# Performance work log

Hardware: AMD Instinct MI355X
Metric: run time of the kernel (lower is better)

Reference implementation:

```python
import jax, jax.numpy as jnp
import numpy as np

DIM = 1024
T = 16384
WINDOW = 32
DIM_HEAD = 64
HEADS = DIM // DIM_HEAD  # 16
EPS = 1e-5


def setup_inputs() -> dict:
    key = jax.random.key(0)
    k1, k2, k3 = jax.random.split(key, 3)
    x = jax.random.normal(k1, (DIM, T), dtype=jnp.float32)
    w_qkv = jax.random.normal(k2, (3 * DIM, DIM), dtype=jnp.float32) / np.float32(np.sqrt(DIM))
    w_out = jax.random.normal(k3, (DIM, DIM), dtype=jnp.float32) / np.float32(np.sqrt(DIM))
    gamma = jnp.ones((DIM,), dtype=jnp.float32)
    beta = jnp.zeros((DIM,), dtype=jnp.float32)
    return {"x": x, "w_qkv": w_qkv, "w_out": w_out, "gamma": gamma, "beta": beta}


def _rotate_half(t):
    # original: split channels into (2, d/2), swap halves with negation
    d = t.shape[-1]
    return jnp.concatenate((-t[..., d // 2:], t[..., :d // 2]), axis=-1)


def reference(x, w_qkv, w_out, gamma, beta):
    C, Tn = x.shape
    xt = x.T  # (T, C)
    # LayerNorm over channel dim (eqx.nn.LayerNorm, eps=1e-5)
    mu = jnp.mean(xt, axis=-1, keepdims=True)
    var = jnp.var(xt, axis=-1, keepdims=True)
    normed = (xt - mu) * jax.lax.rsqrt(var + EPS) * gamma + beta
    # QKV projection (Linear with weight (out,in), no bias)
    qkv = normed @ w_qkv.T  # (T, 3C)
    q, k, v = jnp.split(qkv, 3, axis=-1)
    w = Tn // WINDOW
    def towin(t):  # (w n) (h d) -> h w n d
        return t.reshape(w, WINDOW, HEADS, DIM_HEAD).transpose(2, 0, 1, 3)
    q, k, v = map(towin, (q, k, v))
    # rotary pos emb over window positions (use_xpos=False -> scale == 1)
    inv_freq = 1.0 / (10000.0 ** (jnp.arange(0, DIM_HEAD, 2, dtype=jnp.float32) / DIM_HEAD))
    tpos = jnp.arange(WINDOW, dtype=jnp.float32)
    freqs = jnp.einsum('i,j->ij', tpos, inv_freq)  # (n, d/2)
    freqs = jnp.concatenate((freqs, freqs), axis=-1)  # (n, d)
    cos, sin = jnp.cos(freqs), jnp.sin(freqs)
    q = q * cos + _rotate_half(q) * sin
    k = k * cos + _rotate_half(k) * sin
    # per-head, per-window full (non-causal) attention
    scale = DIM_HEAD ** -0.5
    logits = jnp.einsum('hwnd,hwmd->hwnm', q, k) * scale
    attn = jax.nn.softmax(logits, axis=-1)
    out = jnp.einsum('hwnm,hwmd->hwnd', attn, v)
    out = out.transpose(1, 2, 0, 3).reshape(Tn, C)  # h w n d -> (w n) (h d)
    out = out @ w_out.T
    return out.T + x
```

## Files before the change

### kernel.cpp

```cpp
#include <hip/hip_runtime.h>

#define T_TOK 16384
#define C_DIM 1024

typedef float f32x4 __attribute__((ext_vector_type(4)));
typedef float f32x16 __attribute__((ext_vector_type(16)));
typedef __bf16 bf16x8 __attribute__((ext_vector_type(8)));
typedef unsigned short u16x8 __attribute__((ext_vector_type(8)));
typedef unsigned short u16x4 __attribute__((ext_vector_type(4)));

__device__ __forceinline__ unsigned short f2bf(float f) {
  union { float f; unsigned u; } v; v.f = f;
  unsigned r = v.u + 0x7fffu + ((v.u >> 16) & 1u);
  return (unsigned short)(r >> 16);
}
__device__ __forceinline__ float bf2f(unsigned short h) {
  union { unsigned u; float f; } v; v.u = ((unsigned)h) << 16;
  return v.f;
}
__device__ __forceinline__ unsigned pk2(float a, float b) {
  return (unsigned)f2bf(a) | ((unsigned)f2bf(b) << 16);
}

__global__ __launch_bounds__(256) void cvt_kernel(const float* __restrict__ in,
                                                  unsigned short* __restrict__ out, int n4) {
  int i = blockIdx.x * 256 + threadIdx.x;
  if (i >= n4) return;
  f32x4 v = *(const f32x4*)(in + (size_t)i * 4);
  u16x4 o;
#pragma unroll
  for (int j = 0; j < 4; ++j) o[j] = f2bf(v[j]);
  *(u16x4*)(out + (size_t)i * 4) = o;
}

__global__ __launch_bounds__(256) void rope_tab_kernel(float* __restrict__ tab) {
  int idx = blockIdx.x * 256 + threadIdx.x;
  if (idx >= 1024) return;
  int mm = idx >> 5, d = idx & 31;
  float invf = powf(10000.f, -(float)d * (1.f / 32.f));
  float ang = (float)mm * invf;
  float s, c;
  sincosf(ang, &s, &c);
  tab[idx * 2] = c;
  tab[idx * 2 + 1] = s;
}

__global__ __launch_bounds__(256) void ln_fused_kernel(const float* __restrict__ x,
                                                       const float* __restrict__ gamma,
                                                       const float* __restrict__ beta,
                                                       unsigned short* __restrict__ normed) {
  __shared__ float tile[1024][33];
  __shared__ float s1[8][32], s2[8][32];
  __shared__ float ms[32], rs[32];
  const int tid = threadIdx.x;
  const int t0 = blockIdx.x * 32;

  {
    const int tok = tid & 31, g = tid >> 5;
    float s = 0.f, ss = 0.f;
    const float* p = x + (size_t)(g * 128) * T_TOK + t0 + tok;
#pragma unroll 4
    for (int i = 0; i < 128; ++i) {
      float v = p[(size_t)i * T_TOK];
      tile[g * 128 + i][tok] = v;
      s += v; ss += v * v;
    }
    s1[g][tok] = s; s2[g][tok] = ss;
  }
  __syncthreads();
  if (tid < 32) {
    float S = 0.f, SS = 0.f;
#pragma unroll
    for (int g = 0; g < 8; ++g) { S += s1[g][tid]; SS += s2[g][tid]; }
    float m = S * (1.f / 1024.f);
    float var = SS * (1.f / 1024.f) - m * m;
    ms[tid] = m;
    rs[tid] = rsqrtf(var + 1e-5f);
  }
  __syncthreads();

  {
    const int tok = tid >> 3, cg = tid & 7;
    const float m = ms[tok], rr = rs[tok];
#pragma unroll
    for (int i = 0; i < 16; ++i) {
      int ch8 = cg * 8 + i * 64;
      u16x8 o;
#pragma unroll
      for (int j = 0; j < 8; ++j) {
        float v = tile[ch8 + j][tok];
        o[j] = f2bf((v - m) * rr * gamma[ch8 + j] + beta[ch8 + j]);
      }
      *(u16x8*)&normed[(size_t)(t0 + tok) * C_DIM + ch8] = o;
    }
  }
}

#define GLDS(gp, lp) \
  __builtin_amdgcn_global_load_lds((const __attribute__((address_space(1))) void*)(gp), \
                                   (__attribute__((address_space(3))) void*)(lp), 16, 0, 0)

#define BARF() do { __builtin_amdgcn_s_barrier(); asm volatile("" ::: "memory"); } while (0)
#define VMC(n) asm volatile("s_waitcnt vmcnt(" #n ")" ::: "memory")

__global__ __launch_bounds__(512, 2) void qkvattn_kernel(const unsigned short* __restrict__ A,
                                                         const unsigned short* __restrict__ Bq,
                                                         const float* __restrict__ ropeT,
                                                         unsigned short* __restrict__ aout) {
  __shared__ unsigned short arena[57344];
  unsigned short* LA = arena;
  unsigned short* LB = arena + 32768;
  unsigned short* QKl = arena;
  unsigned short* Vtl = arena + 34816;

  const int tid = threadIdx.x;
  const int w = tid >> 6, lane = tid & 63;
  const int wm = w >> 1, wn = w & 1;
  const int K = 1024, KT = 16;

  const int xcd = blockIdx.x & 7;
  const int ib = blockIdx.x >> 3;
  const int tt = xcd * 8 + (ib & 7);
  const int h = ib >> 3;
  const size_t m0 = (size_t)tt * 256;

  const int preslot = ((lane & 7) ^ (lane >> 3)) * 8;
  const unsigned short* gA = A + (m0 + w * 8 + (lane >> 3)) * (size_t)K + preslot;
  const unsigned short* gB0 = Bq + ((size_t)(0 + h * 64 + w * 8 + (lane >> 3))) * K + preslot;
  const unsigned short* gB1 = Bq + ((size_t)(1024 + h * 64 + w * 8 + (lane >> 3))) * K + preslot;
  const unsigned short* gB2 = Bq + ((size_t)(2048 + h * 64 + w * 8 + (lane >> 3))) * K + preslot;

  auto stageA4 = [&](int b, int kt) {
    const size_t k0 = (size_t)kt * 64;
    GLDS(gA + k0,                   LA + b * 16384 + (w * 8) * 64);
    GLDS(gA + (size_t)64 * K + k0,  LA + b * 16384 + (64 + w * 8) * 64);
    GLDS(gA + (size_t)128 * K + k0, LA + b * 16384 + (128 + w * 8) * 64);
    GLDS(gA + (size_t)192 * K + k0, LA + b * 16384 + (192 + w * 8) * 64);
  };
  auto stageB3 = [&](int b, int kt) {
    const size_t k0 = (size_t)kt * 64;
    GLDS(gB0 + k0, LB + b * 12288 + (w * 8) * 64);
    GLDS(gB1 + k0, LB + b * 12288 + (64 + w * 8) * 64);
    GLDS(gB2 + k0, LB + b * 12288 + (128 + w * 8) * 64);
  };

  f32x4 acc[4][6];
#pragma unroll
  for (int i = 0; i < 4; ++i)
#pragma unroll
    for (int j = 0; j < 6; ++j) acc[i][j] = (f32x4){0.f, 0.f, 0.f, 0.f};

  const int off_r = (lane & 15) * 64;
  const int slot0 = (((lane >> 4) ^ (lane & 7)) * 8);
  const int slot1 = slot0 ^ 32;

  bf16x8 aF[4][2], bF[6][2];

  stageA4(0, 0); stageB3(0, 0);
  stageA4(1, 1); stageB3(1, 1);
  VMC(7);
  BARF();

  int bb = 0;
  for (int t = 0; t < KT; ++t, bb ^= 1) {
    const unsigned short* Ab = LA + bb * 16384 + (wm * 64) * 64;
    const unsigned short* Bb = LB + bb * 12288 + (wn * 96) * 64;

#pragma unroll
    for (int mi = 0; mi < 2; ++mi) {
      aF[mi][0] = *(const bf16x8*)&Ab[mi * 1024 + off_r + slot0];
      aF[mi][1] = *(const bf16x8*)&Ab[mi * 1024 + off_r + slot1];
    }
#pragma unroll
    for (int ni = 0; ni < 6; ++ni) {
      bF[ni][0] = *(const bf16x8*)&Bb[ni * 1024 + off_r + slot0];
      bF[ni][1] = *(const bf16x8*)&Bb[ni * 1024 + off_r + slot1];
    }

    __builtin_amdgcn_s_setprio(1);
#pragma unroll
    for (int mi = 0; mi < 2; ++mi)
#pragma unroll
      for (int ni = 0; ni < 3; ++ni)
#pragma unroll
        for (int ks = 0; ks < 2; ++ks)
          acc[mi][ni] = __builtin_amdgcn_mfma_f32_16x16x32_bf16(aF[mi][ks], bF[ni][ks], acc[mi][ni], 0, 0, 0);
    __builtin_amdgcn_s_setprio(0);

#pragma unroll
    for (int mi = 2; mi < 4; ++mi) {
      aF[mi][0] = *(const bf16x8*)&Ab[mi * 1024 + off_r + slot0];
      aF[mi][1] = *(const bf16x8*)&Ab[mi * 1024 + off_r + slot1];
    }

    __builtin_amdgcn_s_setprio(1);
#pragma unroll
    for (int mi = 0; mi < 2; ++mi)
#pragma unroll
      for (int ni = 3; ni < 6; ++ni)
#pragma unroll
        for (int ks = 0; ks < 2; ++ks)
          acc[mi][ni] = __builtin_amdgcn_mfma_f32_16x16x32_bf16(aF[mi][ks], bF[ni][ks], acc[mi][ni], 0, 0, 0);
    __builtin_amdgcn_s_setprio(0);
    BARF();

    if (t + 2 < KT) stageB3(bb, t + 2);

    __builtin_amdgcn_s_setprio(1);
#pragma unroll
    for (int mi = 2; mi < 4; ++mi)
#pragma unroll
      for (int ni = 3; ni < 6; ++ni)
#pragma unroll
        for (int ks = 0; ks < 2; ++ks)
          acc[mi][ni] = __builtin_amdgcn_mfma_f32_16x16x32_bf16(aF[mi][ks], bF[ni][ks], acc[mi][ni], 0, 0, 0);
    __builtin_amdgcn_s_setprio(0);
    BARF();

    if (t + 2 < KT) stageA4(bb, t + 2);

    __builtin_amdgcn_s_setprio(1);
#pragma unroll
    for (int mi = 2; mi < 4; ++mi)
#pragma unroll
      for (int ni = 0; ni < 3; ++ni)
#pragma unroll
        for (int ks = 0; ks < 2; ++ks)
          acc[mi][ni] = __builtin_amdgcn_mfma_f32_16x16x32_bf16(aF[mi][ks], bF[ni][ks], acc[mi][ni], 0, 0, 0);
    __builtin_amdgcn_s_setprio(0);

    if (t + 2 < KT) {
      VMC(7);
    } else {
      VMC(0);
    }
    BARF();
  }

  __syncthreads();
#pragma unroll
  for (int mi = 0; mi < 4; ++mi)
#pragma unroll
    for (int ni = 0; ni < 6; ++ni) {
      const int j = wn * 96 + ni * 16 + (lane & 15);
#pragma unroll
      for (int r = 0; r < 4; ++r) {
        int tok = wm * 64 + mi * 16 + (lane >> 4) * 4 + r;
        unsigned short bv = f2bf(acc[mi][ni][r]);
        if (wn == 0 || ni < 2) {
          QKl[tok * 136 + j] = bv;
        } else {
          int d = j - 128;
          int mm = tok & 31, win = tok >> 5;
          Vtl[(win * 64 + d) * 32 + ((((mm >> 3) ^ (d ^ (d >> 2))) & 3) * 8 + (mm & 7))] = bv;
        }
      }
    }
  __syncthreads();

  {
    const int m = lane & 31, hi = lane >> 5;
    const unsigned short* qp = QKl + (size_t)(w * 32 + m) * 136;
    u16x8 qv[4], kv[4];
#pragma unroll
    for (int s = 0; s < 4; ++s) {
      int off = s * 16 + hi * 8;
      qv[s] = *(const u16x8*)(qp + off);
      kv[s] = *(const u16x8*)(qp + 64 + off);
    }

    f32x4 ct[2][4];
    const float* tp = ropeT + (size_t)(m * 32 + hi * 8) * 2;
#pragma unroll
    for (int kp = 0; kp < 2; ++kp)
#pragma unroll
      for (int q = 0; q < 4; ++q)
        ct[kp][q] = *(const f32x4*)(tp + kp * 32 + q * 4);

    union FU { unsigned u[4]; bf16x8 v; };
    bf16x8 qfr[4], kfr[4];
#pragma unroll
    for (int ks = 0; ks < 4; ++ks) {
      const int kp = ks & 1;
      FU fq, fk;
#pragma unroll
      for (int jp = 0; jp < 4; ++jp) {
        float c0 = ct[kp][jp][0], s0 = ct[kp][jp][1];
        float c1 = ct[kp][jp][2], s1 = ct[kp][jp][3];
        float q0 = bf2f(qv[ks][2 * jp]), q1 = bf2f(qv[ks][2 * jp + 1]);
        float k0 = bf2f(kv[ks][2 * jp]), k1 = bf2f(kv[ks][2 * jp + 1]);
        float rq0, rq1, rk0, rk1;
        if (ks < 2) {
          rq0 = -bf2f(qv[ks + 2][2 * jp]); rq1 = -bf2f(qv[ks + 2][2 * jp + 1]);
          rk0 = -bf2f(kv[ks + 2][2 * jp]); rk1 = -bf2f(kv[ks + 2][2 * jp + 1]);
        } else {
          rq0 = bf2f(qv[ks - 2][2 * jp]); rq1 = bf2f(qv[ks - 2][2 * jp + 1]);
          rk0 = bf2f(kv[ks - 2][2 * jp]); rk1 = bf2f(kv[ks - 2][2 * jp + 1]);
        }
        fq.u[jp] = pk2(q0 * c0 + rq0 * s0, q1 * c1 + rq1 * s1);
        fk.u[jp] = pk2(k0 * c0 + rk0 * s0, k1 * c1 + rk1 * s1);
      }
      qfr[ks] = fq.v; kfr[ks] = fk.v;
    }

    f32x16 accS;
#pragma unroll
    for (int i = 0; i < 16; ++i) accS[i] = 0.f;
#pragma unroll
    for (int ks = 0; ks < 4; ++ks)
      accS = __builtin_amdgcn_mfma_f32_32x32x16_bf16(kfr[ks], qfr[ks], accS, 0, 0, 0);

    float p[16];
    float mx = -1e30f;
#pragma unroll
    for (int r = 0; r < 16; ++r) { p[r] = accS[r] * 0.125f; mx = fmaxf(mx, p[r]); }
    mx = fmaxf(mx, __shfl_xor(mx, 32, 64));
    float sum = 0.f;
#pragma unroll
    for (int r = 0; r < 16; ++r) { p[r] = __expf(p[r] - mx); sum += p[r]; }
    sum += __shfl_xor(sum, 32, 64);
    const float inv = 1.f / sum;
#pragma unroll
    for (int r = 0; r < 16; ++r) p[r] *= inv;

    bf16x8 pfr[2];
    {
      FU f0, f1;
      unsigned a0 = hi ? pk2(p[0], p[1]) : pk2(p[4], p[5]);
      unsigned a1 = hi ? pk2(p[2], p[3]) : pk2(p[6], p[7]);
      unsigned b0 = (unsigned)__shfl_xor((int)a0, 32, 64);
      unsigned b1 = (unsigned)__shfl_xor((int)a1, 32, 64);
      if (hi) { f0.u[0] = b0; f0.u[1] = b1; f0.u[2] = pk2(p[4], p[5]); f0.u[3] = pk2(p[6], p[7]); }
      else    { f0.u[0] = pk2(p[0], p[1]); f0.u[1] = pk2(p[2], p[3]); f0.u[2] = b0; f0.u[3] = b1; }
      unsigned a2 = hi ? pk2(p[8], p[9])   : pk2(p[12], p[13]);
      unsigned a3 = hi ? pk2(p[10], p[11]) : pk2(p[14], p[15]);
      unsigned b2 = (unsigned)__shfl_xor((int)a2, 32, 64);
      unsigned b3 = (unsigned)__shfl_xor((int)a3, 32, 64);
      if (hi) { f1.u[0] = b2; f1.u[1] = b3; f1.u[2] = pk2(p[12], p[13]); f1.u[3] = pk2(p[14], p[15]); }
      else    { f1.u[0] = pk2(p[8], p[9]); f1.u[1] = pk2(p[10], p[11]); f1.u[2] = b2; f1.u[3] = b3; }
      pfr[0] = f0.v; pfr[1] = f1.v;
    }

    f32x16 accO[2];
#pragma unroll
    for (int i = 0; i < 16; ++i) { accO[0][i] = 0.f; accO[1][i] = 0.f; }
    const int dl = lane & 31;
#pragma unroll
    for (int dh = 0; dh < 2; ++dh) {
      int d = dh * 32 + dl;
      int sx = (d ^ (d >> 2)) & 3;
#pragma unroll
      for (int ks = 0; ks < 2; ++ks) {
        bf16x8 vf = *(const bf16x8*)&Vtl[(w * 64 + d) * 32 + (((2 * ks + hi) ^ sx) & 3) * 8];
        accO[dh] = __builtin_amdgcn_mfma_f32_32x32x16_bf16(pfr[ks], vf, accO[dh], 0, 0, 0);
      }
    }

    const int W = tt * 8 + w;
#pragma unroll
    for (int r = 0; r < 16; ++r) {
      int n = (r & 3) + 8 * (r >> 2) + 4 * hi;
      size_t o = (size_t)(W * 32 + n) * 1024 + h * 64 + dl;
      aout[o] = f2bf(accO[0][r]);
      aout[o + 32] = f2bf(accO[1][r]);
    }
  }
}

template <int EPI>
__global__ __launch_bounds__(512, 2) void gemm8p_kernel(const unsigned short* __restrict__ A,
                                                        const unsigned short* __restrict__ B,
                                                        unsigned short* __restrict__ Obf,
                                                        int ldo, int nbn, int K,
                                                        const float* __restrict__ Xadd,
                                                        float* __restrict__ Ofp) {
  __shared__ unsigned short Lds[2][2][2][8192];
  const int tid = threadIdx.x;
  const int w = tid >> 6, lane = tid & 63;
  const int wm = w >> 2, wn = w & 3;

  const int nbm = gridDim.x / nbn;
  const int xcd = blockIdx.x & 7;
  const int ib = blockIdx.x >> 3;
  int mt, nt;
  if ((nbm & 7) == 0) {
    const int mtpx = nbm >> 3;
    mt = xcd * mtpx + (ib % mtpx);
    nt = ib / mtpx;
  } else {
    const int ntpx = nbn >> 3;
    nt = xcd * ntpx + (ib % ntpx);
    mt = ib / ntpx;
  }
  const size_t m0 = (size_t)mt * 256, n0 = (size_t)nt * 256;

  const unsigned short* gA = A + (m0 + (lane >> 3)) * (size_t)K + ((lane & 7) ^ (lane >> 3)) * 8;
  const unsigned short* gB = B + (n0 + (lane >> 3)) * (size_t)K + ((lane & 7) ^ (lane >> 3)) * 8;
  const int wrow = w * 8;

  auto stageA = [&](int b, int h, int kt) {
    const unsigned short* g = gA + (size_t)(h * 128) * K + (size_t)kt * 64;
    GLDS(g + (size_t)wrow * K,        &Lds[0][b][h][wrow * 64]);
    GLDS(g + (size_t)(64 + wrow) * K, &Lds[0][b][h][(64 + wrow) * 64]);
  };
  auto stageB = [&](int b, int h, int kt) {
    const unsigned short* g = gB + (size_t)(h * 128) * K + (size_t)kt * 64;
    GLDS(g + (size_t)wrow * K,        &Lds[1][b][h][wrow * 64]);
    GLDS(g + (size_t)(64 + wrow) * K, &Lds[1][b][h][(64 + wrow) * 64]);
  };

  f32x4 acc[8][4];
#pragma unroll
  for (int i = 0; i < 8; ++i)
#pragma unroll
    for (int j = 0; j < 4; ++j) acc[i][j] = (f32x4){0.f, 0.f, 0.f, 0.f};

  const int KT = K >> 6;
  const int off_r = (lane & 15) * 64;
  const int slot0 = (((lane >> 4) ^ (lane & 7)) * 8);
  const int slot1 = slot0 ^ 32;
  const int boff = (wn & 1) * 4096;

  bf16x8 aLo[4][2], aHi[4][2], bLo[2][2], bHi[2][2];

  stageA(0, 0, 0); stageA(0, 1, 0); stageB(0, 0, 0); stageB(0, 1, 0);
  if (KT > 1) {
    stageB(1, 0, 1); stageB(1, 1, 1); stageA(1, 0, 1); stageA(1, 1, 1);
    VMC(8);
  } else {
    VMC(0);
  }
  BARF();

  int bb = 0;
  for (int t = 0; t < KT; ++t, bb ^= 1) {
    const unsigned short* Ab = &Lds[0][bb][wm][0];
    const unsigned short* Bb = &Lds[1][bb][wn >> 1][boff];

#pragma unroll
    for (int mi = 0; mi < 4; ++mi) {
      aLo[mi][0] = *(const bf16x8*)&Ab[mi * 1024 + off_r + slot0];
      aLo[mi][1] = *(const bf16x8*)&Ab[mi * 1024 + off_r + slot1];
    }
#pragma unroll
    for (int ni = 0; ni < 2; ++ni) {
      bLo[ni][0] = *(const bf16x8*)&Bb[ni * 1024 + off_r + slot0];
      bLo[ni][1] = *(const bf16x8*)&Bb[ni * 1024 + off_r + slot1];
      bHi[ni][0] = *(const bf16x8*)&Bb[(ni + 2) * 1024 + off_r + slot0];
      bHi[ni][1] = *(const bf16x8*)&Bb[(ni + 2) * 1024 + off_r + slot1];
    }

    __builtin_amdgcn_s_setprio(1);
#pragma unroll
    for (int mi = 0; mi < 4; ++mi)
#pragma unroll
      for (int ni = 0; ni < 2; ++ni)
#pragma unroll
        for (int ks = 0; ks < 2; ++ks)
          acc[mi][ni] = __builtin_amdgcn_mfma_f32_16x16x32_bf16(aLo[mi][ks], bLo[ni][ks], acc[mi][ni], 0, 0, 0);
    __builtin_amdgcn_s_setprio(0);

#pragma unroll
    for (int mi = 0; mi < 4; ++mi) {
      aHi[mi][0] = *(const bf16x8*)&Ab[(mi + 4) * 1024 + off_r + slot0];
      aHi[mi][1] = *(const bf16x8*)&Ab[(mi + 4) * 1024 + off_r + slot1];
    }

    __builtin_amdgcn_s_setprio(1);
#pragma unroll
    for (int mi = 0; mi < 4; ++mi)
#pragma unroll
      for (int ni = 0; ni < 2; ++ni)
#pragma unroll
        for (int ks = 0; ks < 2; ++ks)
          acc[mi][ni + 2] = __builtin_amdgcn_mfma_f32_16x16x32_bf16(aLo[mi][ks], bHi[ni][ks], acc[mi][ni + 2], 0, 0, 0);
    __builtin_amdgcn_s_setprio(0);
    BARF();

    if (t + 2 < KT) { stageB(bb, 0, t + 2); stageB(bb, 1, t + 2); }

    __builtin_amdgcn_s_setprio(1);
#pragma unroll
    for (int mi = 0; mi < 4; ++mi)
#pragma unroll
      for (int ni = 0; ni < 2; ++ni)
#pragma unroll
        for (int ks = 0; ks < 2; ++ks)
          acc[mi + 4][ni + 2] = __builtin_amdgcn_mfma_f32_16x16x32_bf16(aHi[mi][ks], bHi[ni][ks], acc[mi + 4][ni + 2], 0, 0, 0);
    __builtin_amdgcn_s_setprio(0);
    BARF();

    if (t + 2 < KT) { stageA(bb, 0, t + 2); stageA(bb, 1, t + 2); }

    __builtin_amdgcn_s_setprio(1);
#pragma unroll
    for (int mi = 0; mi < 4; ++mi)
#pragma unroll
      for (int ni = 0; ni < 2; ++ni)
#pragma unroll
        for (int ks = 0; ks < 2; ++ks)
          acc[mi + 4][ni] = __builtin_amdgcn_mfma_f32_16x16x32_bf16(aHi[mi][ks], bLo[ni][ks], acc[mi + 4][ni], 0, 0, 0);
    __builtin_amdgcn_s_setprio(0);

    if (t + 2 < KT) {
      VMC(8);
    } else {
      VMC(0);
    }
    BARF();
  }

  if (EPI == 0) {
    unsigned short* cw = &Lds[0][0][0][0] + (size_t)w * 8192;
#pragma unroll
    for (int mi = 0; mi < 8; ++mi)
#pragma unroll
      for (int ni = 0; ni < 4; ++ni)
#pragma unroll
        for (int r = 0; r < 4; ++r)
          cw[(mi * 16 + (lane >> 4) * 4 + r) * 64 + ni * 16 + (lane & 15)] = f2bf(acc[mi][ni][r]);
    const size_t gr0 = m0 + wm * 128;
    const size_t gc0 = n0 + wn * 64;
#pragma unroll
    for (int it = 0; it < 16; ++it) {
      int idx = it * 64 + lane;
      int rr = idx >> 3, c8 = (idx & 7) * 8;
      *(u16x8*)&Obf[(gr0 + rr) * (size_t)ldo + gc0 + c8] = *(const u16x8*)&cw[rr * 64 + c8];
    }
  } else {
    const size_t mrow0 = m0 + wm * 128 + (lane >> 4) * 4;
    const size_t ncol0 = n0 + wn * 64 + (lane & 15);
#pragma unroll
    for (int mi = 0; mi < 8; ++mi)
#pragma unroll
      for (int ni = 0; ni < 4; ++ni)
#pragma unroll
        for (int r = 0; r < 4; ++r) {
          size_t o = (mrow0 + mi * 16 + r) * T_TOK + ncol0 + ni * 16;
          Ofp[o] = acc[mi][ni][r] + Xadd[o];
        }
  }
}

extern "C" void kernel_launch(void* const* d_in, const int* in_sizes, int n_in,
                              void* d_out, int out_size, void* d_ws, size_t ws_size,
                              hipStream_t stream) {
  const float* x     = (const float*)d_in[0];
  const float* w_qkv = (const float*)d_in[1];
  const float* w_out = (const float*)d_in[2];
  const float* gamma = (const float*)d_in[3];
  const float* beta  = (const float*)d_in[4];

  char* ws = (char*)d_ws;
  unsigned short* wqkv_bf = (unsigned short*)(ws);
  unsigned short* wout_bf = (unsigned short*)(ws + 6291456);
  float* ropeT = (float*)(ws + 8519680);
  unsigned short* normed = (unsigned short*)(ws + 8527872);
  unsigned short* aout   = (unsigned short*)(ws + 42082304);

  cvt_kernel<<<3072, 256, 0, stream>>>(w_qkv, wqkv_bf, 3072 * 1024 / 4);
  cvt_kernel<<<1024, 256, 0, stream>>>(w_out, wout_bf, 1024 * 1024 / 4);
  rope_tab_kernel<<<4, 256, 0, stream>>>(ropeT);
  ln_fused_kernel<<<512, 256, 0, stream>>>(x, gamma, beta, normed);
  qkvattn_kernel<<<1024, 512, 0, stream>>>(normed, wqkv_bf, ropeT, aout);
  gemm8p_kernel<1><<<256, 512, 0, stream>>>(wout_bf, aout, nullptr, 0, 64, 1024,
                                            x, (float*)d_out);
}
```

Baseline: 200.3 us.

## Load QKV GEMM A operand directly into registers, bypassing LDS staging

The activation (A) tiles of the fused QKV-attention GEMM are now loaded straight from global memory into register fragments, double-buffered in registers, instead of being staged through LDS. Only the weight (B) tiles still go through LDS, now prefetched one k-tile ahead with a single barrier per tile instead of three. This shrinks the LDS arena and cuts LDS reads and barriers. In exchange, waves that share the same rows load duplicate A data from global memory, register pressure rises, and prefetch depth drops.

```diff
diff --git a/kernel.cpp b/kernel.cpp
--- a/kernel.cpp
+++ b/kernel.cpp
@@ -78,7 +78,6 @@
     rs[tid] = rsqrtf(var + 1e-5f);
   }
   __syncthreads();
-
   {
     const int tok = tid >> 3, cg = tid & 7;
     const float m = ms[tok], rr = rs[tok];
@@ -107,9 +106,8 @@
                                                          const unsigned short* __restrict__ Bq,
                                                          const float* __restrict__ ropeT,
                                                          unsigned short* __restrict__ aout) {
-  __shared__ unsigned short arena[57344];
-  unsigned short* LA = arena;
-  unsigned short* LB = arena + 32768;
+  __shared__ unsigned short arena[51200];
+  unsigned short* LB = arena;
   unsigned short* QKl = arena;
   unsigned short* Vtl = arena + 34816;
 
@@ -125,18 +123,10 @@
   const size_t m0 = (size_t)tt * 256;
 
   const int preslot = ((lane & 7) ^ (lane >> 3)) * 8;
-  const unsigned short* gA = A + (m0 + w * 8 + (lane >> 3)) * (size_t)K + preslot;
   const unsigned short* gB0 = Bq + ((size_t)(0 + h * 64 + w * 8 + (lane >> 3))) * K + preslot;
   const unsigned short* gB1 = Bq + ((size_t)(1024 + h * 64 + w * 8 + (lane >> 3))) * K + preslot;
   const unsigned short* gB2 = Bq + ((size_t)(2048 + h * 64 + w * 8 + (lane >> 3))) * K + preslot;
 
-  auto stageA4 = [&](int b, int kt) {
-    const size_t k0 = (size_t)kt * 64;
-    GLDS(gA + k0,                   LA + b * 16384 + (w * 8) * 64);
-    GLDS(gA + (size_t)64 * K + k0,  LA + b * 16384 + (64 + w * 8) * 64);
-    GLDS(gA + (size_t)128 * K + k0, LA + b * 16384 + (128 + w * 8) * 64);
-    GLDS(gA + (size_t)192 * K + k0, LA + b * 16384 + (192 + w * 8) * 64);
-  };
   auto stageB3 = [&](int b, int kt) {
     const size_t k0 = (size_t)kt * 64;
     GLDS(gB0 + k0, LB + b * 12288 + (w * 8) * 64);
@@ -144,6 +134,15 @@
     GLDS(gB2 + k0, LB + b * 12288 + (128 + w * 8) * 64);
   };
 
+  const unsigned short* gAf = A + (m0 + wm * 64 + (lane & 15)) * (size_t)K + (lane >> 4) * 8;
+  auto loadA = [&](bf16x8 (&dst)[4][2], int kt) {
+#pragma unroll
+    for (int mi = 0; mi < 4; ++mi)
+#pragma unroll
+      for (int ks = 0; ks < 2; ++ks)
+        dst[mi][ks] = *(const bf16x8*)(gAf + (size_t)(mi * 16) * K + kt * 64 + ks * 32);
+  };
+
   f32x4 acc[4][6];
 #pragma unroll
   for (int i = 0; i < 4; ++i)
@@ -154,87 +153,56 @@
   const int slot0 = (((lane >> 4) ^ (lane & 7)) * 8);
   const int slot1 = slot0 ^ 32;
 
-  bf16x8 aF[4][2], bF[6][2];
-
-  stageA4(0, 0); stageB3(0, 0);
-  stageA4(1, 1); stageB3(1, 1);
-  VMC(7);
+  bf16x8 aFA[4][2], aFB[4][2], bF[3][2];
+
+  stageB3(0, 0);
+  loadA(aFA, 0);
+  stageB3(1, 1);
+  VMC(3);
   BARF();
 
-  int bb = 0;
-  for (int t = 0; t < KT; ++t, bb ^= 1) {
-    const unsigned short* Ab = LA + bb * 16384 + (wm * 64) * 64;
-    const unsigned short* Bb = LB + bb * 12288 + (wn * 96) * 64;
-
-#pragma unroll
-    for (int mi = 0; mi < 2; ++mi) {
-      aF[mi][0] = *(const bf16x8*)&Ab[mi * 1024 + off_r + slot0];
-      aF[mi][1] = *(const bf16x8*)&Ab[mi * 1024 + off_r + slot1];
-    }
-#pragma unroll
-    for (int ni = 0; ni < 6; ++ni) {
+  auto tile = [&](int t, int buf, bf16x8 (&aC)[4][2], bf16x8 (&aN)[4][2]) {
+    const unsigned short* Bb = LB + buf * 12288 + (wn * 96) * 64;
+#pragma unroll
+    for (int ni = 0; ni < 3; ++ni) {
       bF[ni][0] = *(const bf16x8*)&Bb[ni * 1024 + off_r + slot0];
       bF[ni][1] = *(const bf16x8*)&Bb[ni * 1024 + off_r + slot1];
     }
-
+    if (t + 1 < KT) { stageB3(buf ^ 1, t + 1); loadA(aN, t + 1); }
     __builtin_amdgcn_s_setprio(1);
 #pragma unroll
-    for (int mi = 0; mi < 2; ++mi)
+    for (int mi = 0; mi < 4; ++mi)
 #pragma unroll
       for (int ni = 0; ni < 3; ++ni)
 #pragma unroll
         for (int ks = 0; ks < 2; ++ks)
-          acc[mi][ni] = __builtin_amdgcn_mfma_f32_16x16x32_bf16(aF[mi][ks], bF[ni][ks], acc[mi][ni], 0, 0, 0);
+          acc[mi][ni] = __builtin_amdgcn_mfma_f32_16x16x32_bf16(aC[mi][ks], bF[ni][ks], acc[mi][ni], 0, 0, 0);
     __builtin_amdgcn_s_setprio(0);
-
-#pragma unroll
-    for (int mi = 2; mi < 4; ++mi) {
-      aF[mi][0] = *(const bf16x8*)&Ab[mi * 1024 + off_r + slot0];
-      aF[mi][1] = *(const bf16x8*)&Ab[mi * 1024 + off_r + slot1];
-    }
-
+#pragma unroll
+    for (int ni = 0; ni < 3; ++ni) {
+      bF[ni][0] = *(const bf16x8*)&Bb[(ni + 3) * 1024 + off_r + slot0];
+      bF[ni][1] = *(const bf16x8*)&Bb[(ni + 3) * 1024 + off_r + slot1];
+    }
     __builtin_amdgcn_s_setprio(1);
 #pragma unroll
-    for (int mi = 0; mi < 2; ++mi)
-#pragma unroll
-      for (int ni = 3; ni < 6; ++ni)
+    for (int mi = 0; mi < 4; ++mi)
+#pragma unroll
+      for (int ni = 0; ni < 3; ++ni)
 #pragma unroll
         for (int ks = 0; ks < 2; ++ks)
-          acc[mi][ni] = __builtin_amdgcn_mfma_f32_16x16x32_bf16(aF[mi][ks], bF[ni][ks], acc[mi][ni], 0, 0, 0);
+          acc[mi][ni + 3] = __builtin_amdgcn_mfma_f32_16x16x32_bf16(aC[mi][ks], bF[ni][ks], acc[mi][ni + 3], 0, 0, 0);
     __builtin_amdgcn_s_setprio(0);
-    BARF();
-
-    if (t + 2 < KT) stageB3(bb, t + 2);
-
-    __builtin_amdgcn_s_setprio(1);
-#pragma unroll
-    for (int mi = 2; mi < 4; ++mi)
-#pragma unroll
-      for (int ni = 3; ni < 6; ++ni)
-#pragma unroll
-        for (int ks = 0; ks < 2; ++ks)
-          acc[mi][ni] = __builtin_amdgcn_mfma_f32_16x16x32_bf16(aF[mi][ks], bF[ni][ks], acc[mi][ni], 0, 0, 0);
-    __builtin_amdgcn_s_setprio(0);
-    BARF();
-
-    if (t + 2 < KT) stageA4(bb, t + 2);
-
-    __builtin_amdgcn_s_setprio(1);
-#pragma unroll
-    for (int mi = 2; mi < 4; ++mi)
-#pragma unroll
-      for (int ni = 0; ni < 3; ++ni)
-#pragma unroll
-        for (int ks = 0; ks < 2; ++ks)
-          acc[mi][ni] = __builtin_amdgcn_mfma_f32_16x16x32_bf16(aF[mi][ks], bF[ni][ks], acc[mi][ni], 0, 0, 0);
-    __builtin_amdgcn_s_setprio(0);
-
-    if (t + 2 < KT) {
-      VMC(7);
+    if (t + 1 < KT) {
+      VMC(8);
     } else {
       VMC(0);
     }
     BARF();
+  };
+
+  for (int tp = 0; tp < KT; tp += 2) {
+    tile(tp, 0, aFA, aFB);
+    tile(tp + 1, 1, aFB, aFA);
   }
 
   __syncthreads();
```

Result: slower. 267.3 us (+33.4%).
